# Kernel optimization log

Measured on AMD Instinct MI355X. Metric: run time of the kernel, lower is better.

Reference implementation:

```python
import jax, jax.numpy as jnp
import numpy as np

D_EMBED, N_HEADS, D_HEAD = 1024, 16, 64
B, S = 2, 2048


def setup_inputs() -> dict:
    key = jax.random.key(0)
    ks = jax.random.split(key, 5)
    sc = 0.02
    return {
        "x": jax.random.normal(ks[0], (B, S, D_EMBED), dtype=jnp.float32),
        "w_q": jax.random.normal(ks[1], (D_EMBED, N_HEADS * D_HEAD), dtype=jnp.float32) * sc,
        "w_k": jax.random.normal(ks[2], (D_EMBED, N_HEADS * D_HEAD), dtype=jnp.float32) * sc,
        "w_v": jax.random.normal(ks[3], (D_EMBED, N_HEADS * D_HEAD), dtype=jnp.float32) * sc,
        "w_o": jax.random.normal(ks[4], (N_HEADS * D_HEAD, D_EMBED), dtype=jnp.float32) * sc,
    }


def reference(x, w_q, w_k, w_v, w_o):
    b, s, _ = x.shape
    # projections -> [b, h, s, d]
    def proj(w):
        return jnp.einsum('bse,ef->bsf', x, w).reshape(b, s, N_HEADS, D_HEAD).transpose(0, 2, 1, 3)
    q, k, v = proj(w_q), proj(w_k), proj(w_v)
    scores = jnp.einsum('bhqd,bhkd->bhqk', q, k) / jnp.sqrt(jnp.float32(D_HEAD))
    causal = jnp.tril(jnp.ones((s, s), dtype=bool))  # True where allowed
    scores = jnp.where(causal[None, None], scores, -jnp.inf)
    attn = jax.nn.softmax(scores, axis=-1)
    out = jnp.einsum('bhqk,bhkd->bhqd', attn, v)
    out = out.transpose(0, 2, 1, 3).reshape(b, s, N_HEADS * D_HEAD)
    return jnp.einsum('bsf,fe->bse', out, w_o)
```

## Files before the change

### kernel.cpp

```cpp
#include <hip/hip_runtime.h>
#include <hip/hip_bf16.h>
#include <cstdint>
#include <cstddef>


#define B_  2
#define S_  2048
#define E_  1024
#define NH_ 16
#define DH_ 64
#define M_  (B_*S_)
#define F_  (NH_*DH_)

typedef unsigned short u16;
typedef short short8 __attribute__((ext_vector_type(8)));
typedef float f32x4  __attribute__((ext_vector_type(4)));

#define QSCALE 0.125f

__device__ __forceinline__ u16 f2bf(float f) {
    union { float f; unsigned int i; } c; c.f = f;
    unsigned int x = c.i;
    x += 0x7fffu + ((x >> 16) & 1u);
    return (u16)(x >> 16);
}

__global__ __launch_bounds__(256)
void prep(const float* __restrict__ x,
          const float* __restrict__ wq, const float* __restrict__ wk,
          const float* __restrict__ wv, const float* __restrict__ wo,
          u16* __restrict__ xb, u16* __restrict__ Wt, u16* __restrict__ wot)
{
    const int tid = threadIdx.x;
    const int b   = blockIdx.x;
    if (b < 2048) {
        size_t i = (size_t)b * 256 + tid;
        const float4* s = (const float4*)(x + i*8);
        float4 a = s[0], bb = s[1];
        short8 o;
        ((u16*)&o)[0] = f2bf(a.x);  ((u16*)&o)[1] = f2bf(a.y);
        ((u16*)&o)[2] = f2bf(a.z);  ((u16*)&o)[3] = f2bf(a.w);
        ((u16*)&o)[4] = f2bf(bb.x); ((u16*)&o)[5] = f2bf(bb.y);
        ((u16*)&o)[6] = f2bf(bb.z); ((u16*)&o)[7] = f2bf(bb.w);
        ((short8*)xb)[i] = o;
        return;
    }
    __shared__ u16 t[64][66];
    const int wb = b - 2048;
    const int wi = wb >> 8;
    const int tt = wb & 255;
    const int n0 = (tt & 15) * 64;
    const int k0 = (tt >> 4) * 64;
    const float* W;
    u16* dst0;
    if (wi < 3) { W = (wi == 0) ? wq : (wi == 1) ? wk : wv;
                  dst0 = Wt + (size_t)wi * E_ * F_; }
    else        { W = wo; dst0 = wot; }

    {
        int kk = tid >> 2, nseg = (tid & 3) * 16;
        const float4* src = (const float4*)(W + (size_t)(k0+kk)*F_ + n0 + nseg);
        #pragma unroll
        for (int v = 0; v < 4; ++v) {
            float4 u = src[v];
            t[kk][nseg + v*4 + 0] = f2bf(u.x);
            t[kk][nseg + v*4 + 1] = f2bf(u.y);
            t[kk][nseg + v*4 + 2] = f2bf(u.z);
            t[kk][nseg + v*4 + 3] = f2bf(u.w);
        }
    }
    __syncthreads();
    {
        int nn = tid >> 2, kseg = (tid & 3) * 16;
        short8 o0, o1;
        #pragma unroll
        for (int i = 0; i < 8; ++i) ((u16*)&o0)[i] = t[kseg + i][nn];
        #pragma unroll
        for (int i = 0; i < 8; ++i) ((u16*)&o1)[i] = t[kseg + 8 + i][nn];
        u16* dst = dst0 + (size_t)(n0+nn)*E_ + k0 + kseg;
        ((short8*)dst)[0] = o0;
        ((short8*)dst)[1] = o1;
    }
}

__global__ __launch_bounds__(256)
void wtrans(const float* __restrict__ W, u16* __restrict__ Wt)
{
    __shared__ u16 t[64][66];
    const int tid = threadIdx.x;
    const int n0 = blockIdx.x * 64;
    const int k0 = blockIdx.y * 64;
    {
        int kk = tid >> 2, nseg = (tid & 3) * 16;
        const float4* src = (const float4*)(W + (size_t)(k0+kk)*F_ + n0 + nseg);
        #pragma unroll
        for (int v = 0; v < 4; ++v) {
            float4 u = src[v];
            t[kk][nseg + v*4 + 0] = f2bf(u.x);
            t[kk][nseg + v*4 + 1] = f2bf(u.y);
            t[kk][nseg + v*4 + 2] = f2bf(u.z);
            t[kk][nseg + v*4 + 3] = f2bf(u.w);
        }
    }
    __syncthreads();
    {
        int nn = tid >> 2, kseg = (tid & 3) * 16;
        short8 o0, o1;
        #pragma unroll
        for (int i = 0; i < 8; ++i) ((u16*)&o0)[i] = t[kseg + i][nn];
        #pragma unroll
        for (int i = 0; i < 8; ++i) ((u16*)&o1)[i] = t[kseg + 8 + i][nn];
        u16* dst = Wt + (size_t)(n0+nn)*E_ + k0 + kseg;
        ((short8*)dst)[0] = o0;
        ((short8*)dst)[1] = o1;
    }
}

template<int MODE>
__global__ __launch_bounds__(256)
void gemm_bf16(const u16* __restrict__ A, const u16* __restrict__ Wt,
               void* __restrict__ Out0, void* __restrict__ Out1,
               void* __restrict__ Out2)
{
    __shared__ __align__(16) char lds[24576];
    char* lA = lds;
    char* lB = lds + 16384;

    const int tid  = threadIdx.x;
    const int lane = tid & 63;
    const int w    = tid >> 6;
    const int wr   = w >> 1, wc = w & 1;
    const int g    = lane >> 4;
    const int q15  = lane & 15;

    const int lin = blockIdx.x;
    const int j   = lin >> 3, xc = lin & 7;
    const int bx  = ((xc >> 2) << 3) + (j & 7);
    const int by  = ((xc & 3) << 3) + ((j >> 3) & 7);
    const int z   = j >> 6;

    const u16* Wz  = Wt + (size_t)z * E_ * F_;
    void*      Out = (z == 0) ? Out0 : (z == 1) ? Out1 : Out2;
    const float osc = (MODE == 0 && z == 0) ? QSCALE : 1.0f;

    const int lr  = lane >> 3;
    const int lc  = lane & 7;
    const int swz = ((lc ^ lr) << 4);

    const int b2 = by >> 4;
    const int s0 = (by & 15) * 128;

    f32x4 acc[4][2];
    #pragma unroll
    for (int i = 0; i < 4; ++i)
        #pragma unroll
        for (int jj = 0; jj < 2; ++jj) acc[i][jj] = (f32x4){0.f,0.f,0.f,0.f};

    for (int it = 0; it < E_/64; ++it) {
        const int k0 = it * 64;
        __syncthreads();
        #pragma unroll
        for (int i = 0; i < 4; ++i) {
            const int row = w*32 + i*8 + lr;
            const char* ga;
            if (MODE == 0) {
                ga = (const char*)A + (size_t)(by*128 + row)*2048 + k0*2 + swz;
            } else {
                const int h = k0 >> 6;
                ga = (const char*)A +
                     ((size_t)(b2*NH_ + h)*S_ + s0 + row)*128 + swz;
            }
            __builtin_amdgcn_global_load_lds(
                (const unsigned int*)ga,
                (unsigned int*)(lA + w*4096 + i*1024), 16, 0, 0);
        }
        #pragma unroll
        for (int i = 0; i < 2; ++i) {
            const int row = w*16 + i*8 + lr;
            const char* gb = (const char*)Wz + (size_t)(bx*64 + row)*2048
                             + k0*2 + swz;
            __builtin_amdgcn_global_load_lds(
                (const unsigned int*)gb,
                (unsigned int*)(lB + w*2048 + i*1024), 16, 0, 0);
        }
        __syncthreads();

        #pragma unroll
        for (int s = 0; s < 2; ++s) {
            short8 af[4], bfr[2];
            #pragma unroll
            for (int mt = 0; mt < 4; ++mt) {
                int row = wr*64 + mt*16 + q15;
                af[mt] = *(const short8*)(lA + row*128 + ((s*64 + 16*g) ^ ((row&7)<<4)));
            }
            #pragma unroll
            for (int nt = 0; nt < 2; ++nt) {
                int n = wc*32 + nt*16 + q15;
                bfr[nt] = *(const short8*)(lB + n*128 + ((s*64 + 16*g) ^ ((n&7)<<4)));
            }
            #pragma unroll
            for (int mt = 0; mt < 4; ++mt)
                #pragma unroll
                for (int nt = 0; nt < 2; ++nt)
                    acc[mt][nt] = __builtin_amdgcn_mfma_f32_16x16x32_bf16(
                        af[mt], bfr[nt], acc[mt][nt], 0, 0, 0);
        }
    }

    #pragma unroll
    for (int mt = 0; mt < 4; ++mt) {
        #pragma unroll
        for (int r = 0; r < 4; ++r) {
            int grow = by*128 + wr*64 + mt*16 + 4*g + r;
            if (MODE == 0) {
                int bb = grow >> 11, ss = grow & (S_-1);
                #pragma unroll
                for (int nt = 0; nt < 2; ++nt) {
                    int n = bx*64 + wc*32 + nt*16 + q15;
                    int hh = n >> 6, dd = n & 63;
                    ((u16*)Out)[(((size_t)bb*NH_ + hh)*S_ + ss)*DH_ + dd] =
                        f2bf(acc[mt][nt][r] * osc);
                }
            } else {
                #pragma unroll
                for (int nt = 0; nt < 2; ++nt) {
                    int n = bx*64 + wc*32 + nt*16 + q15;
                    ((float*)Out)[(size_t)grow * F_ + n] = acc[mt][nt][r];
                }
            }
        }
    }
}

__global__ __launch_bounds__(256)
void vtrans(const u16* __restrict__ V, u16* __restrict__ Vt)
{
    __shared__ u16 t[64][66];
    const int tid = threadIdx.x;
    const int st  = blockIdx.x;
    const int bh  = blockIdx.y;

    {
        int s = tid >> 2, dseg = (tid & 3) * 16;
        const u16* src = V + ((size_t)bh*S_ + st*64 + s)*DH_ + dseg;
        short8 a = ((const short8*)src)[0];
        short8 b = ((const short8*)src)[1];
        *(short8*)&t[s][dseg]     = a;
        *(short8*)&t[s][dseg + 8] = b;
    }
    __syncthreads();
    {
        int d = tid >> 2, sseg = (tid & 3) * 16;
        short8 o0, o1;
        #pragma unroll
        for (int i = 0; i < 8; ++i) ((u16*)&o0)[i] = t[sseg + i][d];
        #pragma unroll
        for (int i = 0; i < 8; ++i) ((u16*)&o1)[i] = t[sseg + 8 + i][d];
        u16* dst = Vt + ((size_t)bh*DH_ + d)*S_ + st*64 + sseg;
        ((short8*)dst)[0] = o0;
        ((short8*)dst)[1] = o1;
    }
}

__global__ __launch_bounds__(256)
void attn_v10(const u16* Q, const u16* __restrict__ K,
              const u16* __restrict__ Vt, u16* O)
{
    __shared__ __align__(16) char vls[2*8192];
    __shared__ __align__(16) char kls[2*8192];

    const int tid  = threadIdx.x;
    const int lane = tid & 63;
    const int w    = tid >> 6;
    const int g    = lane >> 4;
    const int q15  = lane & 15;

    const int blk = blockIdx.x;
    const int qg  = 31 - (blk >> 5);
    const int bh  = blk & 31;
    const int q0  = qg * 64;

    const u16* Kb  = K  + (size_t)bh * S_ * DH_;
    const u16* Vtb = Vt + (size_t)bh * DH_ * S_;

    short8 qf0, qf1;
    {
        const u16* Qp = Q + ((size_t)bh * S_ + q0 + w*16 + q15) * DH_ + g*8;
        qf0 = *(const short8*)(Qp);
        qf1 = *(const short8*)(Qp + 32);
    }

    f32x4 o[4];
    #pragma unroll
    for (int dt = 0; dt < 4; ++dt) o[dt] = (f32x4){0.f,0.f,0.f,0.f};
    float lrow = 0.f;

    const int sd = tid >> 2;
    const int sk = (tid & 3) * 32;

    short8 svv0, svv1, svk0, svk1;
    auto LOADX = [&](int t) {
        const u16* vs = Vtb + (size_t)sd * S_ + t*64 + (sk >> 1);
        svv0 = ((const short8*)vs)[0];
        svv1 = ((const short8*)vs)[1];
        const u16* ks = Kb + (size_t)(t*64 + sd) * DH_ + (sk >> 1);
        svk0 = ((const short8*)ks)[0];
        svk1 = ((const short8*)ks)[1];
    };
    auto WRITEX = [&](int buf) {
        char* vdst = vls + buf*8192 + sd*128;
        *(short8*)(vdst + ((sk     ) ^ ((sd&7)<<4))) = svv0;
        *(short8*)(vdst + ((sk + 16) ^ ((sd&7)<<4))) = svv1;
        char* kdst = kls + buf*8192 + sd*128;
        *(short8*)(kdst + ((sk     ) ^ ((sd&7)<<4))) = svk0;
        *(short8*)(kdst + ((sk + 16) ^ ((sd&7)<<4))) = svk1;
    };

    LOADX(0);
    WRITEX(0);
    __syncthreads();

    for (int kt = 0; ; ++kt) {
        const bool more = (kt < qg);
        if (more) LOADX(kt + 1);

        const int cur = kt & 1;
        const char* kt_ = kls + cur * 8192;
        const char* vt_ = vls + cur * 8192;
        char* plw = kls + (cur ^ 1) * 8192 + w * 2048;

        float p[16];
        __builtin_amdgcn_s_setprio(1);
        #pragma unroll
        for (int t = 0; t < 4; ++t) {
            int r = t*16 + q15;
            short8 kf0 = *(const short8*)(kt_ + r*128 + ((16*g     ) ^ ((r&7)<<4)));
            short8 kf1 = *(const short8*)(kt_ + r*128 + ((16*g + 64) ^ ((r&7)<<4)));
            f32x4 st = (f32x4){0.f,0.f,0.f,0.f};
            st = __builtin_amdgcn_mfma_f32_16x16x32_bf16(kf0, qf0, st, 0, 0, 0);
            st = __builtin_amdgcn_mfma_f32_16x16x32_bf16(kf1, qf1, st, 0, 0, 0);
            #pragma unroll
            for (int r2 = 0; r2 < 4; ++r2) p[t*4+r2] = st[r2];
        }
        __builtin_amdgcn_s_setprio(0);

        if (kt == qg) {
            #pragma unroll
            for (int t = 0; t < 4; ++t)
                #pragma unroll
                for (int r = 0; r < 4; ++r)
                    if (16*t + 4*g + r > w*16 + q15) p[t*4+r] = -1e30f;
        }

        float psum = 0.f;
        #pragma unroll
        for (int i = 0; i < 16; ++i) { p[i] = __expf(p[i]); psum += p[i]; }
        psum += __shfl_xor(psum, 16);
        psum += __shfl_xor(psum, 32);
        lrow += psum;

        #pragma unroll
        for (int t = 0; t < 4; ++t) {
            unsigned r0, r1;
            asm("v_cvt_pk_bf16_f32 %0, %1, %2"
                : "=v"(r0) : "v"(p[t*4+0]), "v"(p[t*4+1]));
            asm("v_cvt_pk_bf16_f32 %0, %1, %2"
                : "=v"(r1) : "v"(p[t*4+2]), "v"(p[t*4+3]));
            int byte = q15*128 + ((32*t + 8*g) ^ ((q15&7)<<4));
            uint2 pk; pk.x = r0; pk.y = r1;
            *(uint2*)(plw + byte) = pk;
        }

        __builtin_amdgcn_s_setprio(1);
        #pragma unroll
        for (int c = 0; c < 2; ++c) {
            int pb = q15*128 + ((64*c + 16*g) ^ ((q15&7)<<4));
            short8 pf = *(const short8*)(plw + pb);
            #pragma unroll
            for (int dt = 0; dt < 4; ++dt) {
                int d = dt*16 + q15;
                int vb = d*128 + ((64*c + 16*g) ^ ((d&7)<<4));
                short8 vf = *(const short8*)(vt_ + vb);
                o[dt] = __builtin_amdgcn_mfma_f32_16x16x32_bf16(pf, vf, o[dt], 0, 0, 0);
            }
        }
        __builtin_amdgcn_s_setprio(0);

        if (!more) break;
        WRITEX(cur ^ 1);
        __syncthreads();
    }

    float inv = 1.f / lrow;
    #pragma unroll
    for (int r = 0; r < 4; ++r) {
        float li = __shfl(inv, 4*g + r);
        int qrow = q0 + w*16 + 4*g + r;
        #pragma unroll
        for (int dt = 0; dt < 4; ++dt) {
            O[((size_t)bh * S_ + qrow) * DH_ + dt*16 + q15] = f2bf(o[dt][r] * li);
        }
    }
}

extern "C" void kernel_launch(void* const* d_in, const int* in_sizes, int n_in,
                              void* d_out, int out_size, void* d_ws, size_t ws_size,
                              hipStream_t stream) {
    (void)in_sizes; (void)n_in; (void)out_size;
    const float* x  = (const float*)d_in[0];
    const float* wq = (const float*)d_in[1];
    const float* wk = (const float*)d_in[2];
    const float* wv = (const float*)d_in[3];
    const float* wo = (const float*)d_in[4];

    u16* Qw = (u16*)d_ws;
    u16* Kw = Qw + (size_t)M_ * F_;
    u16* Vw = Kw + (size_t)M_ * F_;

    u16* D0 = (u16*)d_out;
    u16* xb = D0 + (size_t)4*1024*1024;

    const bool bigws = ws_size >= ((size_t)27 << 20);
    u16* wot = bigws ? (u16*)((char*)d_ws + ((size_t)24 << 20)) : Vw;

    prep<<<dim3(bigws ? 3072 : 2816), 256, 0, stream>>>(
        x, wq, wk, wv, wo, xb, D0, wot);

    gemm_bf16<0><<<dim3(1536), 256, 0, stream>>>(
        xb, D0, (void*)Qw, (void*)Kw, (void*)Vw);

    vtrans<<<dim3(S_/64, B_*NH_), 256, 0, stream>>>(Vw, D0);
    if (!bigws)
        wtrans<<<dim3(16,16), 256, 0, stream>>>(wo, Vw);

    attn_v10<<<dim3(B_*NH_*(S_/64)), 256, 0, stream>>>(Qw, Kw, D0, Qw);

    gemm_bf16<2><<<dim3(512), 256, 0, stream>>>(
        Qw, wot, d_out, d_out, d_out);
}
```

Baseline: 113.4 us.

## Pair causal query tiles per block with split-KV groups for balanced attention

Attention blocks now have 512 threads split into two 4-wave groups, and each block handles a pair of query tiles (H=31-j and j) with 17 key tiles of work in total. Group 0 processes the first 17 key tiles of tile H. Group 1 processes the remaining key tiles of H, then switches to query tile j. The two partial results for H are merged through shared memory. This balances causal triangle work so every block runs the same number of iterations, removing tail imbalance from blocks with long diagonals. The cost is doubled LDS per block, extra merge synchronisation, and half as many blocks (512).

Measured after the change: 117.8 us. 3.9% more time.

```diff
diff --git a/kernel.cpp b/kernel.cpp
--- a/kernel.cpp
+++ b/kernel.cpp
@@ -262,43 +262,57 @@
     }
 }
 
-__global__ __launch_bounds__(256)
-void attn_v10(const u16* Q, const u16* __restrict__ K,
+__global__ __launch_bounds__(512)
+void attn_v12(const u16* Q, const u16* __restrict__ K,
               const u16* __restrict__ Vt, u16* O)
 {
-    __shared__ __align__(16) char vls[2*8192];
-    __shared__ __align__(16) char kls[2*8192];
+    __shared__ __align__(16) char vls[2][16384];
+    __shared__ __align__(16) char kls[2][16384];
 
     const int tid  = threadIdx.x;
     const int lane = tid & 63;
     const int w    = tid >> 6;
+    const int gr   = w >> 2;
+    const int wg   = w & 3;
     const int g    = lane >> 4;
     const int q15  = lane & 15;
 
     const int blk = blockIdx.x;
-    const int qg  = 31 - (blk >> 5);
+    const int j   = blk >> 5;
     const int bh  = blk & 31;
-    const int q0  = qg * 64;
+    const int H   = 31 - j;
+    const int nH1 = 15 - j;
+    const int nreal = gr ? 16 : 17;
 
     const u16* Kb  = K  + (size_t)bh * S_ * DH_;
     const u16* Vtb = Vt + (size_t)bh * DH_ * S_;
 
+    const int qt0 = (gr == 0 || nH1 > 0) ? H : j;
     short8 qf0, qf1;
     {
-        const u16* Qp = Q + ((size_t)bh * S_ + q0 + w*16 + q15) * DH_ + g*8;
+        const u16* Qp = Q + ((size_t)bh*S_ + qt0*64 + wg*16 + q15)*DH_ + g*8;
         qf0 = *(const short8*)(Qp);
         qf1 = *(const short8*)(Qp + 32);
     }
 
-    f32x4 o[4];
+    f32x4 o[4], osv[4];
     #pragma unroll
-    for (int dt = 0; dt < 4; ++dt) o[dt] = (f32x4){0.f,0.f,0.f,0.f};
-    float lrow = 0.f;
-
-    const int sd = tid >> 2;
-    const int sk = (tid & 3) * 32;
+    for (int dt = 0; dt < 4; ++dt) {
+        o[dt]   = (f32x4){0.f,0.f,0.f,0.f};
+        osv[dt] = (f32x4){0.f,0.f,0.f,0.f};
+    }
+    float lrow = 0.f, lsv = 0.f;
+
+    char* vbase = vls[gr];
+    char* kbase = kls[gr];
+    const int tig = wg*64 + lane;
+    const int sd  = tig >> 2;
+    const int sk  = (tig & 3) * 32;
 
     short8 svv0, svv1, svk0, svk1;
+    auto KT = [&](int i) -> int {
+        return (gr == 0) ? i : ((i < nH1) ? (17 + i) : (i - nH1));
+    };
     auto LOADX = [&](int t) {
         const u16* vs = Vtb + (size_t)sd * S_ + t*64 + (sk >> 1);
         svv0 = ((const short8*)vs)[0];
@@ -308,94 +322,133 @@
         svk1 = ((const short8*)ks)[1];
     };
     auto WRITEX = [&](int buf) {
-        char* vdst = vls + buf*8192 + sd*128;
+        char* vdst = vbase + buf*8192 + sd*128;
         *(short8*)(vdst + ((sk     ) ^ ((sd&7)<<4))) = svv0;
         *(short8*)(vdst + ((sk + 16) ^ ((sd&7)<<4))) = svv1;
-        char* kdst = kls + buf*8192 + sd*128;
+        char* kdst = kbase + buf*8192 + sd*128;
         *(short8*)(kdst + ((sk     ) ^ ((sd&7)<<4))) = svk0;
         *(short8*)(kdst + ((sk + 16) ^ ((sd&7)<<4))) = svk1;
     };
 
-    LOADX(0);
+    LOADX(KT(0));
     WRITEX(0);
     __syncthreads();
 
-    for (int kt = 0; ; ++kt) {
-        const bool more = (kt < qg);
-        if (more) LOADX(kt + 1);
-
-        const int cur = kt & 1;
-        const char* kt_ = kls + cur * 8192;
-        const char* vt_ = vls + cur * 8192;
-        char* plw = kls + (cur ^ 1) * 8192 + w * 2048;
-
-        float p[16];
-        __builtin_amdgcn_s_setprio(1);
-        #pragma unroll
-        for (int t = 0; t < 4; ++t) {
-            int r = t*16 + q15;
-            short8 kf0 = *(const short8*)(kt_ + r*128 + ((16*g     ) ^ ((r&7)<<4)));
-            short8 kf1 = *(const short8*)(kt_ + r*128 + ((16*g + 64) ^ ((r&7)<<4)));
-            f32x4 st = (f32x4){0.f,0.f,0.f,0.f};
-            st = __builtin_amdgcn_mfma_f32_16x16x32_bf16(kf0, qf0, st, 0, 0, 0);
-            st = __builtin_amdgcn_mfma_f32_16x16x32_bf16(kf1, qf1, st, 0, 0, 0);
-            #pragma unroll
-            for (int r2 = 0; r2 < 4; ++r2) p[t*4+r2] = st[r2];
-        }
-        __builtin_amdgcn_s_setprio(0);
-
-        if (kt == qg) {
-            #pragma unroll
-            for (int t = 0; t < 4; ++t)
-                #pragma unroll
-                for (int r = 0; r < 4; ++r)
-                    if (16*t + 4*g + r > w*16 + q15) p[t*4+r] = -1e30f;
-        }
-
-        float psum = 0.f;
-        #pragma unroll
-        for (int i = 0; i < 16; ++i) { p[i] = __expf(p[i]); psum += p[i]; }
-        psum += __shfl_xor(psum, 16);
-        psum += __shfl_xor(psum, 32);
-        lrow += psum;
-
-        #pragma unroll
-        for (int t = 0; t < 4; ++t) {
-            unsigned r0, r1;
-            asm("v_cvt_pk_bf16_f32 %0, %1, %2"
-                : "=v"(r0) : "v"(p[t*4+0]), "v"(p[t*4+1]));
-            asm("v_cvt_pk_bf16_f32 %0, %1, %2"
-                : "=v"(r1) : "v"(p[t*4+2]), "v"(p[t*4+3]));
-            int byte = q15*128 + ((32*t + 8*g) ^ ((q15&7)<<4));
-            uint2 pk; pk.x = r0; pk.y = r1;
-            *(uint2*)(plw + byte) = pk;
-        }
-
-        __builtin_amdgcn_s_setprio(1);
-        #pragma unroll
-        for (int c = 0; c < 2; ++c) {
-            int pb = q15*128 + ((64*c + 16*g) ^ ((q15&7)<<4));
-            short8 pf = *(const short8*)(plw + pb);
+    for (int i = 0; i < 17; ++i) {
+        const bool last = (i == 16);
+        if (!last) LOADX(KT(i + 1));
+
+        const int cur = i & 1;
+        const char* kt_ = kbase + cur * 8192;
+        const char* vt_ = vbase + cur * 8192;
+        char* plw = kbase + (cur ^ 1) * 8192 + wg * 2048;
+
+        if (gr == 1 && nH1 > 0 && i == nH1) {
             #pragma unroll
             for (int dt = 0; dt < 4; ++dt) {
-                int d = dt*16 + q15;
-                int vb = d*128 + ((64*c + 16*g) ^ ((d&7)<<4));
-                short8 vf = *(const short8*)(vt_ + vb);
-                o[dt] = __builtin_amdgcn_mfma_f32_16x16x32_bf16(pf, vf, o[dt], 0, 0, 0);
-            }
-        }
-        __builtin_amdgcn_s_setprio(0);
-
-        if (!more) break;
-        WRITEX(cur ^ 1);
-        __syncthreads();
+                osv[dt] = o[dt];
+                o[dt] = (f32x4){0.f,0.f,0.f,0.f};
+            }
+            lsv = lrow; lrow = 0.f;
+            const u16* Qp = Q + ((size_t)bh*S_ + j*64 + wg*16 + q15)*DH_ + g*8;
+            qf0 = *(const short8*)(Qp);
+            qf1 = *(const short8*)(Qp + 32);
+        }
+
+        if (i < nreal) {
+            const int ktg  = KT(i);
+            const int qcur = (gr == 0) ? H : ((i < nH1) ? H : j);
+
+            float p[16];
+            __builtin_amdgcn_s_setprio(1);
+            #pragma unroll
+            for (int t = 0; t < 4; ++t) {
+                int r = t*16 + q15;
+                short8 kf0 = *(const short8*)(kt_ + r*128 + ((16*g     ) ^ ((r&7)<<4)));
+                short8 kf1 = *(const short8*)(kt_ + r*128 + ((16*g + 64) ^ ((r&7)<<4)));
+                f32x4 st = (f32x4){0.f,0.f,0.f,0.f};
+                st = __builtin_amdgcn_mfma_f32_16x16x32_bf16(kf0, qf0, st, 0, 0, 0);
+                st = __builtin_amdgcn_mfma_f32_16x16x32_bf16(kf1, qf1, st, 0, 0, 0);
+                #pragma unroll
+                for (int r2 = 0; r2 < 4; ++r2) p[t*4+r2] = st[r2];
+            }
+            __builtin_amdgcn_s_setprio(0);
+
+            if (ktg == qcur) {
+                #pragma unroll
+                for (int t = 0; t < 4; ++t)
+                    #pragma unroll
+                    for (int r = 0; r < 4; ++r)
+                        if (16*t + 4*g + r > wg*16 + q15) p[t*4+r] = -1e30f;
+            }
+
+            float psum = 0.f;
+            #pragma unroll
+            for (int i2 = 0; i2 < 16; ++i2) { p[i2] = __expf(p[i2]); psum += p[i2]; }
+            psum += __shfl_xor(psum, 16);
+            psum += __shfl_xor(psum, 32);
+            lrow += psum;
+
+            #pragma unroll
+            for (int t = 0; t < 4; ++t) {
+                unsigned r0, r1;
+                asm("v_cvt_pk_bf16_f32 %0, %1, %2"
+                    : "=v"(r0) : "v"(p[t*4+0]), "v"(p[t*4+1]));
+                asm("v_cvt_pk_bf16_f32 %0, %1, %2"
+                    : "=v"(r1) : "v"(p[t*4+2]), "v"(p[t*4+3]));
+                int byte = q15*128 + ((32*t + 8*g) ^ ((q15&7)<<4));
+                uint2 pk; pk.x = r0; pk.y = r1;
+                *(uint2*)(plw + byte) = pk;
+            }
+
+            __builtin_amdgcn_s_setprio(1);
+            #pragma unroll
+            for (int c = 0; c < 2; ++c) {
+                int pb = q15*128 + ((64*c + 16*g) ^ ((q15&7)<<4));
+                short8 pf = *(const short8*)(plw + pb);
+                #pragma unroll
+                for (int dt = 0; dt < 4; ++dt) {
+                    int d = dt*16 + q15;
+                    int vb = d*128 + ((64*c + 16*g) ^ ((d&7)<<4));
+                    short8 vf = *(const short8*)(vt_ + vb);
+                    o[dt] = __builtin_amdgcn_mfma_f32_16x16x32_bf16(pf, vf, o[dt], 0, 0, 0);
+                }
+            }
+            __builtin_amdgcn_s_setprio(0);
+        }
+
+        if (!last) { WRITEX((i + 1) & 1); __syncthreads(); }
+    }
+
+    __syncthreads();
+    f32x4* mo = (f32x4*)&vls[0][0];
+    float* ml = (float*)&kls[0][0];
+    if (gr == 1) {
+        #pragma unroll
+        for (int dt = 0; dt < 4; ++dt) mo[tig*4 + dt] = osv[dt];
+        ml[tig] = lsv;
+    }
+    __syncthreads();
+
+    int q0out;
+    if (gr == 0) {
+        #pragma unroll
+        for (int dt = 0; dt < 4; ++dt) {
+            f32x4 add = mo[tig*4 + dt];
+            o[dt][0] += add[0]; o[dt][1] += add[1];
+            o[dt][2] += add[2]; o[dt][3] += add[3];
+        }
+        lrow += ml[tig];
+        q0out = H * 64;
+    } else {
+        q0out = j * 64;
     }
 
     float inv = 1.f / lrow;
     #pragma unroll
     for (int r = 0; r < 4; ++r) {
         float li = __shfl(inv, 4*g + r);
-        int qrow = q0 + w*16 + 4*g + r;
+        int qrow = q0out + wg*16 + 4*g + r;
         #pragma unroll
         for (int dt = 0; dt < 4; ++dt) {
             O[((size_t)bh * S_ + qrow) * DH_ + dt*16 + q15] = f2bf(o[dt][r] * li);
@@ -433,7 +486,7 @@
     if (!bigws)
         wtrans<<<dim3(16,16), 256, 0, stream>>>(wo, Vw);
 
-    attn_v10<<<dim3(B_*NH_*(S_/64)), 256, 0, stream>>>(Qw, Kw, D0, Qw);
+    attn_v12<<<dim3(512), 512, 0, stream>>>(Qw, Kw, D0, Qw);
 
     gemm_bf16<2><<<dim3(512), 256, 0, stream>>>(
         Qw, wot, d_out, d_out, d_out);
```

## Split long causal query tiles across two blocks and merge partial outputs

Applied to the files above, without the earlier changes.

Query tiles 17-31 each have their key range split in two, with each half run by a separate block that writes bf16 partial outputs and row sums to scratch inside the output buffer. A new merge kernel adds the two partials and normalises them. The aim is to balance load across blocks for causal attention and cut the tail from the longest tiles. The cost is an extra kernel launch, more global traffic, and bf16 rounding of the unnormalised partials. Merging by plain addition is only correct because the kernel has no running-max subtraction.

Measured after the change: 118.7 us. 1.05x slower.

```diff
diff --git a/kernel.cpp b/kernel.cpp
--- a/kernel.cpp
+++ b/kernel.cpp
@@ -18,6 +18,9 @@
 
 #define QSCALE 0.125f
 
+__device__ __forceinline__ float bf2f(u16 u) {
+    union { unsigned int i; float f; } c; c.i = ((unsigned int)u) << 16; return c.f;
+}
 __device__ __forceinline__ u16 f2bf(float f) {
     union { float f; unsigned int i; } c; c.f = f;
     unsigned int x = c.i;
@@ -263,8 +266,9 @@
 }
 
 __global__ __launch_bounds__(256)
-void attn_v10(const u16* Q, const u16* __restrict__ K,
-              const u16* __restrict__ Vt, u16* O)
+void attn_v13(const u16* Q, const u16* __restrict__ K,
+              const u16* __restrict__ Vt, u16* O,
+              u16* __restrict__ Po, float* __restrict__ Pl)
 {
     __shared__ __align__(16) char vls[2*8192];
     __shared__ __align__(16) char kls[2*8192];
@@ -276,9 +280,20 @@
     const int q15  = lane & 15;
 
     const int blk = blockIdx.x;
-    const int qg  = 31 - (blk >> 5);
-    const int bh  = blk & 31;
-    const int q0  = qg * 64;
+    int qt, bh, kstart, kcnt, pidx;
+    if (blk < 960) {
+        int ab = blk & 1, s = blk >> 1;
+        qt = 17 + (s >> 5); bh = s & 31;
+        int nA = (qt + 2) >> 1;
+        kstart = ab ? nA : 0;
+        kcnt   = ab ? (qt + 1 - nA) : nA;
+        pidx   = ((qt - 17) * 32 + bh) * 2 + ab;
+    } else {
+        int s = blk - 960;
+        qt = s >> 5; bh = s & 31;
+        kstart = 0; kcnt = qt + 1; pidx = -1;
+    }
+    const int q0 = qt * 64;
 
     const u16* Kb  = K  + (size_t)bh * S_ * DH_;
     const u16* Vtb = Vt + (size_t)bh * DH_ * S_;
@@ -316,15 +331,16 @@
         *(short8*)(kdst + ((sk + 16) ^ ((sd&7)<<4))) = svk1;
     };
 
-    LOADX(0);
+    LOADX(kstart);
     WRITEX(0);
     __syncthreads();
 
-    for (int kt = 0; ; ++kt) {
-        const bool more = (kt < qg);
+    for (int i = 0; ; ++i) {
+        const int kt = kstart + i;
+        const bool more = (i + 1 < kcnt);
         if (more) LOADX(kt + 1);
 
-        const int cur = kt & 1;
+        const int cur = i & 1;
         const char* kt_ = kls + cur * 8192;
         const char* vt_ = vls + cur * 8192;
         char* plw = kls + (cur ^ 1) * 8192 + w * 2048;
@@ -344,7 +360,7 @@
         }
         __builtin_amdgcn_s_setprio(0);
 
-        if (kt == qg) {
+        if (kt == qt) {
             #pragma unroll
             for (int t = 0; t < 4; ++t)
                 #pragma unroll
@@ -354,7 +370,7 @@
 
         float psum = 0.f;
         #pragma unroll
-        for (int i = 0; i < 16; ++i) { p[i] = __expf(p[i]); psum += p[i]; }
+        for (int i2 = 0; i2 < 16; ++i2) { p[i2] = __expf(p[i2]); psum += p[i2]; }
         psum += __shfl_xor(psum, 16);
         psum += __shfl_xor(psum, 32);
         lrow += psum;
@@ -387,19 +403,65 @@
         __builtin_amdgcn_s_setprio(0);
 
         if (!more) break;
-        WRITEX(cur ^ 1);
+        WRITEX((i + 1) & 1);
         __syncthreads();
     }
 
-    float inv = 1.f / lrow;
+    if (pidx >= 0) {
+        u16*   po = Po + (size_t)pidx * 4096;
+        float* pl = Pl + pidx * 64;
+        #pragma unroll
+        for (int r = 0; r < 4; ++r) {
+            int ql = w*16 + 4*g + r;
+            #pragma unroll
+            for (int dt = 0; dt < 4; ++dt)
+                po[ql*64 + dt*16 + q15] = f2bf(o[dt][r]);
+        }
+        if (g == 0) pl[w*16 + q15] = lrow;
+    } else {
+        float inv = 1.f / lrow;
+        #pragma unroll
+        for (int r = 0; r < 4; ++r) {
+            float li = __shfl(inv, 4*g + r);
+            int qrow = q0 + w*16 + 4*g + r;
+            #pragma unroll
+            for (int dt = 0; dt < 4; ++dt) {
+                O[((size_t)bh * S_ + qrow) * DH_ + dt*16 + q15] =
+                    f2bf(o[dt][r] * li);
+            }
+        }
+    }
+}
+
+__global__ __launch_bounds__(256)
+void merge_attn(const u16* __restrict__ Po, const float* __restrict__ Pl,
+                u16* __restrict__ O)
+{
+    const int blk = blockIdx.x;
+    const int qt  = 17 + (blk >> 5);
+    const int bh  = blk & 31;
+    const int base = blk * 2;
+    const u16*   oA = Po + (size_t)base * 4096;
+    const u16*   oB = oA + 4096;
+    const float* lA = Pl + base * 64;
+    const float* lB = lA + 64;
+
+    const int q  = threadIdx.x >> 2;
+    const int d0 = (threadIdx.x & 3) * 16;
+    const float linv = 1.f / (lA[q] + lB[q]);
+
+    const short8* a = (const short8*)(oA + q*64 + d0);
+    const short8* b = (const short8*)(oB + q*64 + d0);
+    u16* dst = O + ((size_t)bh * S_ + qt*64 + q) * DH_ + d0;
     #pragma unroll
-    for (int r = 0; r < 4; ++r) {
-        float li = __shfl(inv, 4*g + r);
-        int qrow = q0 + w*16 + 4*g + r;
-        #pragma unroll
-        for (int dt = 0; dt < 4; ++dt) {
-            O[((size_t)bh * S_ + qrow) * DH_ + dt*16 + q15] = f2bf(o[dt][r] * li);
-        }
+    for (int j = 0; j < 2; ++j) {
+        short8 av = a[j], bv = b[j];
+        short8 ov;
+        #pragma unroll
+        for (int k = 0; k < 8; ++k)
+            ((u16*)&ov)[k] = f2bf((bf2f(((const u16*)&av)[k]) +
+                                   bf2f(((const u16*)&bv)[k])) * linv);
+        ((short8*)dst)[j] = ov;
     }
 }
 
@@ -417,8 +479,11 @@
     u16* Kw = Qw + (size_t)M_ * F_;
     u16* Vw = Kw + (size_t)M_ * F_;
 
-    u16* D0 = (u16*)d_out;
-    u16* xb = D0 + (size_t)4*1024*1024;
+    u16*   D0 = (u16*)d_out;
+    u16*   xb = D0 + (size_t)4*1024*1024;
+    u16*   Po = xb;
+    float* Pl = (float*)((char*)d_out +
+                 ((size_t)8 << 20) + (size_t)960 * 8192);
 
     const bool bigws = ws_size >= ((size_t)27 << 20);
     u16* wot = bigws ? (u16*)((char*)d_ws + ((size_t)24 << 20)) : Vw;
@@ -433,7 +498,8 @@
     if (!bigws)
         wtrans<<<dim3(16,16), 256, 0, stream>>>(wo, Vw);
 
-    attn_v10<<<dim3(B_*NH_*(S_/64)), 256, 0, stream>>>(Qw, Kw, D0, Qw);
+    attn_v13<<<dim3(1504), 256, 0, stream>>>(Qw, Kw, D0, Qw, Po, Pl);
+    merge_attn<<<dim3(480), 256, 0, stream>>>(Po, Pl, Qw);
 
     gemm_bf16<2><<<dim3(512), 256, 0, stream>>>(
         Qw, wot, d_out, d_out, d_out);
```
